# Kernel optimization log

Measured on AMD Instinct MI355X. Metric: run time of the kernel, lower is better.

The kernel has to match this reference:

```python
import jax, jax.numpy as jnp
import numpy as np
import math

B, L, DIM, H = 2, 2048, 512, 8


def setup_inputs() -> dict:
    key = jax.random.key(0)
    ks = jax.random.split(key, 8)
    s = 0.02
    return {
        "x": jax.random.normal(ks[0], (B, L, DIM), dtype=jnp.float32),
        "Wq": jax.random.normal(ks[1], (DIM, DIM), dtype=jnp.float32) * s,
        "Wk": jax.random.normal(ks[2], (DIM, DIM), dtype=jnp.float32) * s,
        "Wv": jax.random.normal(ks[3], (DIM, DIM), dtype=jnp.float32) * s,
        "Wb": jax.random.normal(ks[4], (H, DIM), dtype=jnp.float32) * s,   # content_bias weight
        "mixing": jax.random.normal(ks[5], (H, DIM), dtype=jnp.float32) * 0.2,  # UNIFORM init, std=0.2
        "Wd": jax.random.normal(ks[6], (DIM, DIM), dtype=jnp.float32) * s,
        "bd": jax.random.normal(ks[7], (DIM,), dtype=jnp.float32) * s,
    }


def reference(x, Wq, Wk, Wv, Wb, mixing, Wd, bd):
    b, l, d = x.shape
    h = mixing.shape[0]
    dh = d // h
    q = x @ Wq.T                      # [B,L,D]
    k = x @ Wk.T                      # [B,S,D]
    v = (x @ Wv.T).reshape(b, l, h, dh).transpose(0, 2, 1, 3)  # [B,H,S,dh]
    # scores[b,h,l,s] = sum_d q[b,l,d] * mixing[h,d] * k[b,s,d]
    scores = jnp.einsum("bld,hd,bsd->bhls", q, mixing, k)
    # content bias: [B,S,H] -> broadcast over query positions as [B,H,1,S]
    cb = jnp.einsum("bsd,hd->bhs", x, Wb)
    scale = math.sqrt(d / h)  # attention_head_size = dim / num_heads
    scores = (scores + cb[:, :, None, :]) / scale
    probs = jax.nn.softmax(scores, axis=-1)   # dropout disabled (eval)
    ctx = jnp.einsum("bhls,bhsd->bhld", probs, v)  # [B,H,L,dh]
    ctx = ctx.transpose(0, 2, 1, 3).reshape(b, l, d)
    return ctx @ Wd.T + bd
```

## Files before the change

### kernel.cpp

```cpp
#include <hip/hip_runtime.h>

#define B_ 2
#define L_ 2048
#define D_ 512
#define H_ 8
#define S_ 2048

typedef __attribute__((ext_vector_type(8))) short short8;
typedef __attribute__((ext_vector_type(8))) unsigned short ushort8;
typedef __attribute__((ext_vector_type(4))) unsigned short ushort4v;
typedef __attribute__((ext_vector_type(4))) float f32x4;
typedef __attribute__((ext_vector_type(16))) float f32x16;
typedef __attribute__((ext_vector_type(4))) float float4v;

__device__ __forceinline__ unsigned short f2bf(float f) {
    unsigned u = __float_as_uint(f);
    u += 0x7FFF + ((u >> 16) & 1);
    return (unsigned short)(u >> 16);
}
__device__ __forceinline__ float bf2f(unsigned short s) {
    return __uint_as_float(((unsigned)s) << 16);
}
__device__ __forceinline__ int swap23(int x) {
    return (x & ~12) | ((x & 4) << 1) | ((x & 8) >> 1);
}
__device__ __forceinline__ void async16(void* lds, const void* g) {
    __builtin_amdgcn_global_load_lds(
        (const __attribute__((address_space(1))) void*)(g),
        (__attribute__((address_space(3))) void*)(lds), 16, 0, 0);
}

__global__ __launch_bounds__(256) void cvt_all(const float* __restrict__ x,
                                               const float* __restrict__ w0, const float* __restrict__ w1,
                                               const float* __restrict__ w2, const float* __restrict__ w3,
                                               unsigned short* __restrict__ xb,
                                               unsigned short* __restrict__ d0, unsigned short* __restrict__ d1,
                                               unsigned short* __restrict__ d2, unsigned short* __restrict__ d3) {
    int i = blockIdx.x * 256 + threadIdx.x;
    const float* s;
    unsigned short* d;
    int idx;
    if (i < 524288) { s = x; d = xb; idx = i; }
    else {
        int off = i - 524288;
        int wsel = off >> 16; idx = off & 65535;
        s = (wsel == 0) ? w0 : (wsel == 1) ? w1 : (wsel == 2) ? w2 : w3;
        d = (wsel == 0) ? d0 : (wsel == 1) ? d1 : (wsel == 2) ? d2 : d3;
    }
    float4v v = *(const float4v*)(s + (size_t)idx * 4);
    ushort4v o;
    o[0] = f2bf(v[0]); o[1] = f2bf(v[1]); o[2] = f2bf(v[2]); o[3] = f2bf(v[3]);
    *(ushort4v*)(d + (size_t)idx * 4) = o;
}

__global__ __launch_bounds__(256) void cb_kernel(const float* __restrict__ x,
                                                 const float* __restrict__ Wb,
                                                 float* __restrict__ cb) {
    const int tid = threadIdx.x, w = tid >> 6, lane = tid & 63;
    const int row = blockIdx.x * 4 + w;
    const int h = lane >> 3, seg = lane & 7;
    const float* xp = x + (size_t)row * 512 + seg * 64;
    const float* wp = Wb + (size_t)h * 512 + seg * 64;
    float acc = 0.f;
    #pragma unroll
    for (int j = 0; j < 16; ++j) {
        float4v xv = *(const float4v*)(xp + j * 4);
        float4v wv = *(const float4v*)(wp + j * 4);
        acc += xv[0] * wv[0] + xv[1] * wv[1] + xv[2] * wv[2] + xv[3] * wv[3];
    }
    acc += __shfl_xor(acc, 1);
    acc += __shfl_xor(acc, 2);
    acc += __shfl_xor(acc, 4);
    if (seg == 0) {
        int b = row >> 11, s = row & 2047;
        cb[((size_t)(b * H_ + h)) * S_ + s] = acc * 0.125f;
    }
}

__device__ __forceinline__ void gemm128_core(const unsigned short* __restrict__ Ap,
                                             const unsigned short* __restrict__ Bp,
                                             short* sA, short* sB, int tid, f32x4 c[4][4]) {
    const int w = tid >> 6, lane = tid & 63, quad = lane >> 4, l15 = lane & 15;
    const int wm = (w >> 1) * 64, wn = (w & 1) * 64;
    for (int kc = 0; kc < 8; ++kc) {
        __syncthreads();
        #pragma unroll
        for (int j = 0; j < 4; ++j) {
            int i = tid + j * 256;
            int row = i >> 3, seg = i & 7;
            *(ushort8*)&sA[row * 72 + seg * 8] = *(const ushort8*)(Ap + (size_t)row * 512 + kc * 64 + seg * 8);
            *(ushort8*)&sB[row * 72 + seg * 8] = *(const ushort8*)(Bp + (size_t)row * 512 + kc * 64 + seg * 8);
        }
        __syncthreads();
        #pragma unroll
        for (int ks = 0; ks < 2; ++ks) {
            short8 a[4], b[4];
            #pragma unroll
            for (int ii = 0; ii < 4; ++ii)
                a[ii] = *(const short8*)&sA[(wm + ii * 16 + l15) * 72 + ks * 32 + quad * 8];
            #pragma unroll
            for (int jj = 0; jj < 4; ++jj)
                b[jj] = *(const short8*)&sB[(wn + jj * 16 + l15) * 72 + ks * 32 + quad * 8];
            #pragma unroll
            for (int ii = 0; ii < 4; ++ii)
                #pragma unroll
                for (int jj = 0; jj < 4; ++jj)
                    c[ii][jj] = __builtin_amdgcn_mfma_f32_16x16x32_bf16(a[ii], b[jj], c[ii][jj], 0, 0, 0);
        }
    }
}

__global__ __launch_bounds__(256) void gemm_qkv(const unsigned short* __restrict__ xb,
                                                const unsigned short* __restrict__ Wqb,
                                                const unsigned short* __restrict__ Wkb,
                                                const unsigned short* __restrict__ Wvb,
                                                unsigned short* __restrict__ qb,
                                                unsigned short* __restrict__ kpack,
                                                unsigned short* __restrict__ vt) {
    __shared__ short sA[128 * 72];
    __shared__ short sB[128 * 72];
    const int m0 = blockIdx.x * 128, n0 = blockIdx.y * 128, z = blockIdx.z;
    const unsigned short* Bsel = (z == 0) ? Wqb : ((z == 1) ? Wkb : Wvb);
    f32x4 c[4][4];
    #pragma unroll
    for (int ii = 0; ii < 4; ++ii)
        #pragma unroll
        for (int jj = 0; jj < 4; ++jj) { f32x4 zv = {0.f, 0.f, 0.f, 0.f}; c[ii][jj] = zv; }
    gemm128_core(xb + (size_t)m0 * 512, Bsel + (size_t)n0 * 512, sA, sB, threadIdx.x, c);
    const int tid = threadIdx.x, w = tid >> 6, lane = tid & 63, quad = lane >> 4, l15 = lane & 15;
    const int wm = (w >> 1) * 64, wn = (w & 1) * 64;
    #pragma unroll
    for (int ii = 0; ii < 4; ++ii) {
        const int mb = m0 + wm + ii * 16 + quad * 4;
        const int bb = mb >> 11;
        if (z == 0) {
            #pragma unroll
            for (int jj = 0; jj < 4; ++jj) {
                int ncol = n0 + wn + jj * 16 + l15;
                #pragma unroll
                for (int r = 0; r < 4; ++r)
                    qb[(size_t)(mb + r) * 512 + ncol] = f2bf(c[ii][jj][r]);
            }
        } else if (z == 1) {
            #pragma unroll
            for (int jj = 0; jj < 4; ++jj) {
                int d = n0 + wn + jj * 16 + l15;
                int f = d >> 4, hid = (d >> 3) & 1, jq = d & 7;
                #pragma unroll
                for (int r = 0; r < 4; ++r) {
                    int s = (mb + r) & 2047;
                    int t = s >> 5, rr = swap23(s & 31);
                    kpack[(((size_t)(bb * 64 + t)) * 32 + f) * 512 + hid * 256 + rr * 8 + jq]
                        = f2bf(c[ii][jj][r]);
                }
            }
        } else {
            const int hh = (n0 + wn) >> 6;
            const int s = mb & 2047;
            #pragma unroll
            for (int jj = 0; jj < 4; ++jj) {
                int dh = jj * 16 + l15;
                ushort4v o;
                o[0] = f2bf(c[ii][jj][0]); o[1] = f2bf(c[ii][jj][1]);
                o[2] = f2bf(c[ii][jj][2]); o[3] = f2bf(c[ii][jj][3]);
                *(ushort4v*)(vt + (((size_t)(bb * H_ + hh) * 64 + dh) * S_ + s)) = o;
            }
        }
    }
}

__global__ __launch_bounds__(256) void gemm_out(const unsigned short* __restrict__ ctxb,
                                                const unsigned short* __restrict__ Wdb,
                                                const float* __restrict__ bd,
                                                float* __restrict__ out) {
    __shared__ short sA[128 * 72];
    __shared__ short sB[128 * 72];
    const int m0 = blockIdx.x * 128, n0 = blockIdx.y * 128;
    f32x4 c[4][4];
    #pragma unroll
    for (int ii = 0; ii < 4; ++ii)
        #pragma unroll
        for (int jj = 0; jj < 4; ++jj) { f32x4 zv = {0.f, 0.f, 0.f, 0.f}; c[ii][jj] = zv; }
    gemm128_core(ctxb + (size_t)m0 * 512, Wdb + (size_t)n0 * 512, sA, sB, threadIdx.x, c);
    const int tid = threadIdx.x, w = tid >> 6, lane = tid & 63, quad = lane >> 4, l15 = lane & 15;
    const int wm = (w >> 1) * 64, wn = (w & 1) * 64;
    #pragma unroll
    for (int ii = 0; ii < 4; ++ii) {
        const int mb = m0 + wm + ii * 16 + quad * 4;
        #pragma unroll
        for (int jj = 0; jj < 4; ++jj) {
            int ncol = n0 + wn + jj * 16 + l15;
            float bias = bd[ncol];
            #pragma unroll
            for (int r = 0; r < 4; ++r)
                out[(size_t)(mb + r) * 512 + ncol] = c[ii][jj][r] + bias;
        }
    }
}

__global__ __launch_bounds__(256, 2) void flash_attn(const unsigned short* __restrict__ qb,
                                                     const unsigned short* __restrict__ kpack,
                                                     const unsigned short* __restrict__ vt,
                                                     const float* __restrict__ cb_all,
                                                     const float* __restrict__ mixing,
                                                     _Float16* __restrict__ Opart,
                                                     float* __restrict__ lpart) {
    __shared__ short sK[2][8192];
    __shared__ short sV[2048];
    const int bid = blockIdx.x;
    const int half = bid & 1, b = (bid >> 1) & 1, h = (bid >> 2) & 7, qt = bid >> 5;
    const int tid = threadIdx.x, w = tid >> 6, lane = tid & 63;
    const int l31 = lane & 31, hi = lane >> 5;
    const int q0 = qt * 128 + w * 32;
    const unsigned short* kbase = kpack + ((size_t)(b * 64 + half * 32)) * 32 * 512;
    const unsigned short* vtb = vt + ((size_t)(b * H_ + h) * 64) * (size_t)S_;
    const float* cbp = cb_all + (size_t)(b * H_ + h) * S_ + half * 1024;
    const float* mixh = mixing + h * D_;

    short8 qf[32];
    {
        const unsigned short* qrow = qb + ((size_t)(b * L_) + q0 + l31) * D_ + hi * 8;
        #pragma unroll
        for (int i = 0; i < 32; ++i) {
            ushort8 qv = *(const ushort8*)(qrow + i * 16);
            float4v ma = *(const float4v*)(mixh + i * 16 + hi * 8);
            float4v mb = *(const float4v*)(mixh + i * 16 + hi * 8 + 4);
            short8 ov;
            ov[0] = (short)f2bf(bf2f(qv[0]) * ma[0]);
            ov[1] = (short)f2bf(bf2f(qv[1]) * ma[1]);
            ov[2] = (short)f2bf(bf2f(qv[2]) * ma[2]);
            ov[3] = (short)f2bf(bf2f(qv[3]) * ma[3]);
            ov[4] = (short)f2bf(bf2f(qv[4]) * mb[0]);
            ov[5] = (short)f2bf(bf2f(qv[5]) * mb[1]);
            ov[6] = (short)f2bf(bf2f(qv[6]) * mb[2]);
            ov[7] = (short)f2bf(bf2f(qv[7]) * mb[3]);
            qf[i] = ov;
        }
    }

    f32x16 acco0, acco1;
    #pragma unroll
    for (int i = 0; i < 16; ++i) { acco0[i] = 0.f; acco1[i] = 0.f; }
    float lsum = 0.f;

    #pragma unroll
    for (int ii = 0; ii < 4; ++ii)
        async16((char*)&sK[0][0] + w * 1024 + ii * 4096,
                (const char*)kbase + w * 1024 + ii * 4096 + (size_t)lane * 16);
    __syncthreads();

    for (int t = 0; t < 32; ++t) {
        f32x16 accsA, accsB;
        #pragma unroll
        for (int i = 0; i < 16; ++i) { accsA[i] = 0.f; accsB[i] = 0.f; }

        {
            const char* src = (const char*)(kbase + ((size_t)t * 32 + 16) * 512);
            #pragma unroll
            for (int ii = 0; ii < 4; ++ii)
                async16((char*)&sK[1][0] + w * 1024 + ii * 4096,
                        src + w * 1024 + ii * 4096 + (size_t)lane * 16);
            const unsigned short* gv = vtb + ((size_t)((w >> 1) * 32 + l31)) * (size_t)S_
                                       + half * 1024 + t * 32 + (w & 1) * 16 + hi * 8;
            async16((char*)&sV[0] + w * 1024, gv);
        }
        #pragma unroll
        for (int f = 0; f < 16; ++f) {
            short8 a = *(const short8*)&sK[0][f * 512 + lane * 8];
            if (f & 1) accsB = __builtin_amdgcn_mfma_f32_32x32x16_bf16(a, qf[f], accsB, 0, 0, 0);
            else       accsA = __builtin_amdgcn_mfma_f32_32x32x16_bf16(a, qf[f], accsA, 0, 0, 0);
        }
        __syncthreads();

        if (t < 31) {
            const char* src = (const char*)(kbase + ((size_t)(t + 1) * 32) * 512);
            #pragma unroll
            for (int ii = 0; ii < 4; ++ii)
                async16((char*)&sK[0][0] + w * 1024 + ii * 4096,
                        src + w * 1024 + ii * 4096 + (size_t)lane * 16);
        }
        #pragma unroll
        for (int f = 0; f < 16; ++f) {
            short8 a = *(const short8*)&sK[1][f * 512 + lane * 8];
            if (f & 1) accsB = __builtin_amdgcn_mfma_f32_32x32x16_bf16(a, qf[16 + f], accsB, 0, 0, 0);
            else       accsA = __builtin_amdgcn_mfma_f32_32x32x16_bf16(a, qf[16 + f], accsA, 0, 0, 0);
        }

        const int s0 = t * 32;
        float p[16];
        #pragma unroll
        for (int R = 0; R < 16; ++R) {
            const int cr = (R & 3) + 8 * (R >> 2);
            const int idx = s0 + cr - 4 * ((R >> 2) & 1);
            float cbA = cbp[idx];
            float cbB = cbp[idx + 8];
            float cbv = hi ? cbB : cbA;
            float pe = __expf((accsA[R] + accsB[R]) * 0.125f + cbv);
            p[R] = pe;
            lsum += pe;
        }
        union { unsigned int u[4]; short8 s8; } P0, P1;
        #pragma unroll
        for (int j = 0; j < 4; ++j) {
            P0.u[j] = __builtin_amdgcn_perm(__float_as_uint(p[2 * j + 1]) + 0x8000u,
                                            __float_as_uint(p[2 * j]) + 0x8000u, 0x07060302u);
            P1.u[j] = __builtin_amdgcn_perm(__float_as_uint(p[8 + 2 * j + 1]) + 0x8000u,
                                            __float_as_uint(p[8 + 2 * j]) + 0x8000u, 0x07060302u);
        }
        {
            short8 av00 = *(const short8*)&sV[0 * 512 + lane * 8];
            short8 av01 = *(const short8*)&sV[1 * 512 + lane * 8];
            short8 av10 = *(const short8*)&sV[2 * 512 + lane * 8];
            short8 av11 = *(const short8*)&sV[3 * 512 + lane * 8];
            acco0 = __builtin_amdgcn_mfma_f32_32x32x16_bf16(av00, P0.s8, acco0, 0, 0, 0);
            acco0 = __builtin_amdgcn_mfma_f32_32x32x16_bf16(av01, P1.s8, acco0, 0, 0, 0);
            acco1 = __builtin_amdgcn_mfma_f32_32x32x16_bf16(av10, P0.s8, acco1, 0, 0, 0);
            acco1 = __builtin_amdgcn_mfma_f32_32x32x16_bf16(av11, P1.s8, acco1, 0, 0, 0);
        }
        __syncthreads();
    }

    lsum += __shfl_xor(lsum, 32);
    if (hi == 0) lpart[(size_t)bid * 128 + w * 32 + l31] = lsum;
    #pragma unroll
    for (int R = 0; R < 16; ++R) {
        int dh = (R & 3) + 8 * (R >> 2) + 4 * hi;
        Opart[((size_t)bid * 64 + dh) * 128 + w * 32 + l31] = (_Float16)acco0[R];
        Opart[((size_t)bid * 64 + 32 + dh) * 128 + w * 32 + l31] = (_Float16)acco1[R];
    }
}

__global__ __launch_bounds__(256) void merge_ctx(const _Float16* __restrict__ Opart,
                                                 const float* __restrict__ lpart,
                                                 unsigned short* __restrict__ ctxb) {
    int t = blockIdx.x * 256 + threadIdx.x;
    int qq = t & 127, dh4 = (t >> 7) & 15, qt = (t >> 11) & 15, h = (t >> 15) & 7, b = t >> 18;
    int base = (qt << 5) | (h << 2) | (b << 1);
    float l = lpart[(size_t)base * 128 + qq] + lpart[(size_t)(base + 1) * 128 + qq];
    float inv = 1.f / l;
    ushort4v o;
    #pragma unroll
    for (int e = 0; e < 4; ++e) {
        int dh = dh4 * 4 + e;
        float v = (float)Opart[((size_t)base * 64 + dh) * 128 + qq]
                + (float)Opart[((size_t)(base + 1) * 64 + dh) * 128 + qq];
        o[e] = f2bf(v * inv);
    }
    *(ushort4v*)(ctxb + ((size_t)(b * L_) + qt * 128 + qq) * 512 + h * 64 + dh4 * 4) = o;
}

extern "C" void kernel_launch(void* const* d_in, const int* in_sizes, int n_in,
                              void* d_out, int out_size, void* d_ws, size_t ws_size,
                              hipStream_t stream) {
    (void)in_sizes; (void)n_in; (void)out_size; (void)ws_size;
    const float* x      = (const float*)d_in[0];
    const float* Wq     = (const float*)d_in[1];
    const float* Wk     = (const float*)d_in[2];
    const float* Wv     = (const float*)d_in[3];
    const float* Wb     = (const float*)d_in[4];
    const float* mixing = (const float*)d_in[5];
    const float* Wd     = (const float*)d_in[6];
    const float* bd     = (const float*)d_in[7];
    float* out = (float*)d_out;

    char* ws = (char*)d_ws;
    const size_t MiB = 1048576;
    unsigned short* xb    = (unsigned short*)(ws);
    unsigned short* qb    = (unsigned short*)(ws + 4 * MiB);
    unsigned short* kpack = (unsigned short*)(ws + 8 * MiB);
    unsigned short* vt    = (unsigned short*)(ws + 12 * MiB);
    unsigned short* ctxb  = (unsigned short*)(ws + 16 * MiB);
    unsigned short* Wqb   = (unsigned short*)(ws + 20 * MiB);
    unsigned short* Wkb   = (unsigned short*)(ws + 20 * MiB + 512 * 1024);
    unsigned short* Wvb   = (unsigned short*)(ws + 21 * MiB);
    unsigned short* Wdb   = (unsigned short*)(ws + 21 * MiB + 512 * 1024);
    float* cbuf           = (float*)(ws + 22 * MiB);
    float* lpart          = (float*)(ws + 23 * MiB);
    _Float16* Opart       = (_Float16*)(ws + 24 * MiB);

    cvt_all<<<3072, 256, 0, stream>>>(x, Wq, Wk, Wv, Wd, xb, Wqb, Wkb, Wvb, Wdb);
    gemm_qkv<<<dim3(32, 4, 3), 256, 0, stream>>>(xb, Wqb, Wkb, Wvb, qb, kpack, vt);
    cb_kernel<<<1024, 256, 0, stream>>>(x, Wb, cbuf);
    flash_attn<<<512, 256, 0, stream>>>(qb, kpack, vt, cbuf, mixing, Opart, lpart);
    merge_ctx<<<2048, 256, 0, stream>>>(Opart, lpart, ctxb);
    gemm_out<<<dim3(32, 4), 256, 0, stream>>>(ctxb, Wdb, bd, out);
}
```

Baseline: 228.0 us.

## Deepen K/V async prefetch ring to four K and two V buffers

Replaces the two-buffer K and single-buffer V scheme in the flash attention loop with a four-slot K ring and double-buffered V, so loads run further ahead. Full __syncthreads barriers give way to explicit vmcnt waits plus s_barrier. MFMA sections are also wrapped in s_setprio raises to favour matrix issue. This doubles LDS use and relies on hand-counted outstanding-load numbers, which could cost occupancy at 2 blocks per CU or cause races if the counts are wrong.

```diff
diff --git a/kernel.cpp b/kernel.cpp
--- a/kernel.cpp
+++ b/kernel.cpp
@@ -205,8 +205,8 @@
                                                      const float* __restrict__ mixing,
                                                      _Float16* __restrict__ Opart,
                                                      float* __restrict__ lpart) {
-    __shared__ short sK[2][8192];
-    __shared__ short sV[2048];
+    __shared__ short sK[4][8192];
+    __shared__ short sV[2][2048];
     const int bid = blockIdx.x;
     const int half = bid & 1, b = (bid >> 1) & 1, h = (bid >> 2) & 7, qt = bid >> 5;
     const int tid = threadIdx.x, w = tid >> 6, lane = tid & 63;
@@ -237,55 +237,37 @@
             qf[i] = ov;
         }
     }
+    asm volatile("s_waitcnt vmcnt(0)" ::: "memory");
 
     f32x16 acco0, acco1;
     #pragma unroll
     for (int i = 0; i < 16; ++i) { acco0[i] = 0.f; acco1[i] = 0.f; }
     float lsum = 0.f;
-
-    #pragma unroll
-    for (int ii = 0; ii < 4; ++ii)
-        async16((char*)&sK[0][0] + w * 1024 + ii * 4096,
-                (const char*)kbase + w * 1024 + ii * 4096 + (size_t)lane * 16);
-    __syncthreads();
-
-    for (int t = 0; t < 32; ++t) {
-        f32x16 accsA, accsB;
-        #pragma unroll
-        for (int i = 0; i < 16; ++i) { accsA[i] = 0.f; accsB[i] = 0.f; }
-
-        {
-            const char* src = (const char*)(kbase + ((size_t)t * 32 + 16) * 512);
-            #pragma unroll
-            for (int ii = 0; ii < 4; ++ii)
-                async16((char*)&sK[1][0] + w * 1024 + ii * 4096,
-                        src + w * 1024 + ii * 4096 + (size_t)lane * 16);
-            const unsigned short* gv = vtb + ((size_t)((w >> 1) * 32 + l31)) * (size_t)S_
-                                       + half * 1024 + t * 32 + (w & 1) * 16 + hi * 8;
-            async16((char*)&sV[0] + w * 1024, gv);
-        }
+    f32x16 accsA, accsB;
+
+    auto stageK = [&](int p) {
+        const char* src = (const char*)(kbase + (size_t)p * 8192);
+        char* dst = (char*)&sK[p & 3][0];
+        #pragma unroll
+        for (int ii = 0; ii < 4; ++ii)
+            async16(dst + w * 1024 + ii * 4096, src + w * 1024 + ii * 4096 + (size_t)lane * 16);
+    };
+    auto stageV = [&](int u) {
+        const unsigned short* gv = vtb + ((size_t)((w >> 1) * 32 + l31)) * (size_t)S_
+                                   + half * 1024 + u * 32 + (w & 1) * 16 + hi * 8;
+        async16((char*)&sV[u & 1][0] + w * 1024, gv);
+    };
+    auto qk_chunk = [&](const short* buf, int qbase) {
+        __builtin_amdgcn_s_setprio(1);
         #pragma unroll
         for (int f = 0; f < 16; ++f) {
-            short8 a = *(const short8*)&sK[0][f * 512 + lane * 8];
-            if (f & 1) accsB = __builtin_amdgcn_mfma_f32_32x32x16_bf16(a, qf[f], accsB, 0, 0, 0);
-            else       accsA = __builtin_amdgcn_mfma_f32_32x32x16_bf16(a, qf[f], accsA, 0, 0, 0);
-        }
-        __syncthreads();
-
-        if (t < 31) {
-            const char* src = (const char*)(kbase + ((size_t)(t + 1) * 32) * 512);
-            #pragma unroll
-            for (int ii = 0; ii < 4; ++ii)
-                async16((char*)&sK[0][0] + w * 1024 + ii * 4096,
-                        src + w * 1024 + ii * 4096 + (size_t)lane * 16);
-        }
-        #pragma unroll
-        for (int f = 0; f < 16; ++f) {
-            short8 a = *(const short8*)&sK[1][f * 512 + lane * 8];
-            if (f & 1) accsB = __builtin_amdgcn_mfma_f32_32x32x16_bf16(a, qf[16 + f], accsB, 0, 0, 0);
-            else       accsA = __builtin_amdgcn_mfma_f32_32x32x16_bf16(a, qf[16 + f], accsA, 0, 0, 0);
-        }
-
+            short8 a = *(const short8*)&buf[f * 512 + lane * 8];
+            if (f & 1) accsB = __builtin_amdgcn_mfma_f32_32x32x16_bf16(a, qf[qbase + f], accsB, 0, 0, 0);
+            else       accsA = __builtin_amdgcn_mfma_f32_32x32x16_bf16(a, qf[qbase + f], accsA, 0, 0, 0);
+        }
+        __builtin_amdgcn_s_setprio(0);
+    };
+    auto softmax_pv = [&](int t) {
         const int s0 = t * 32;
         float p[16];
         #pragma unroll
@@ -307,17 +289,47 @@
             P1.u[j] = __builtin_amdgcn_perm(__float_as_uint(p[8 + 2 * j + 1]) + 0x8000u,
                                             __float_as_uint(p[8 + 2 * j]) + 0x8000u, 0x07060302u);
         }
-        {
-            short8 av00 = *(const short8*)&sV[0 * 512 + lane * 8];
-            short8 av01 = *(const short8*)&sV[1 * 512 + lane * 8];
-            short8 av10 = *(const short8*)&sV[2 * 512 + lane * 8];
-            short8 av11 = *(const short8*)&sV[3 * 512 + lane * 8];
-            acco0 = __builtin_amdgcn_mfma_f32_32x32x16_bf16(av00, P0.s8, acco0, 0, 0, 0);
-            acco0 = __builtin_amdgcn_mfma_f32_32x32x16_bf16(av01, P1.s8, acco0, 0, 0, 0);
-            acco1 = __builtin_amdgcn_mfma_f32_32x32x16_bf16(av10, P0.s8, acco1, 0, 0, 0);
-            acco1 = __builtin_amdgcn_mfma_f32_32x32x16_bf16(av11, P1.s8, acco1, 0, 0, 0);
-        }
-        __syncthreads();
+        const short* vbuf = &sV[t & 1][0];
+        short8 av00 = *(const short8*)&vbuf[0 * 512 + lane * 8];
+        short8 av01 = *(const short8*)&vbuf[1 * 512 + lane * 8];
+        short8 av10 = *(const short8*)&vbuf[2 * 512 + lane * 8];
+        short8 av11 = *(const short8*)&vbuf[3 * 512 + lane * 8];
+        __builtin_amdgcn_s_setprio(1);
+        acco0 = __builtin_amdgcn_mfma_f32_32x32x16_bf16(av00, P0.s8, acco0, 0, 0, 0);
+        acco0 = __builtin_amdgcn_mfma_f32_32x32x16_bf16(av01, P1.s8, acco0, 0, 0, 0);
+        acco1 = __builtin_amdgcn_mfma_f32_32x32x16_bf16(av10, P0.s8, acco1, 0, 0, 0);
+        acco1 = __builtin_amdgcn_mfma_f32_32x32x16_bf16(av11, P1.s8, acco1, 0, 0, 0);
+        __builtin_amdgcn_s_setprio(0);
+    };
+
+    stageK(0); stageK(1); stageV(0); stageK(2);
+
+    for (int t = 0; t < 31; ++t) {
+        #pragma unroll
+        for (int i = 0; i < 16; ++i) { accsA[i] = 0.f; accsB[i] = 0.f; }
+        const short* be = &sK[(t & 1) << 1][0];
+        const short* bo = &sK[((t & 1) << 1) | 1][0];
+        asm volatile("s_waitcnt vmcnt(9)" ::: "memory");
+        __builtin_amdgcn_s_barrier();
+        stageK(2 * t + 3);
+        qk_chunk(be, 0);
+        asm volatile("s_waitcnt vmcnt(8)" ::: "memory");
+        __builtin_amdgcn_s_barrier();
+        stageV(t + 1);
+        if (t < 30) stageK(2 * t + 4);
+        qk_chunk(bo, 16);
+        softmax_pv(t);
+    }
+    {
+        #pragma unroll
+        for (int i = 0; i < 16; ++i) { accsA[i] = 0.f; accsB[i] = 0.f; }
+        asm volatile("s_waitcnt vmcnt(5)" ::: "memory");
+        __builtin_amdgcn_s_barrier();
+        qk_chunk(&sK[2][0], 0);
+        asm volatile("s_waitcnt vmcnt(0)" ::: "memory");
+        __builtin_amdgcn_s_barrier();
+        qk_chunk(&sK[3][0], 16);
+        softmax_pv(31);
     }
 
     lsum += __shfl_xor(lsum, 32);
```

Result: faster. 210.7 us (-7.6%).
